# Performance work log

Hardware: AMD Instinct MI355X
Metric: run time of the kernel (lower is better)

## Reference

```python
import jax, jax.numpy as jnp
import numpy as np

NUM_ITEMS = 100000
OUT_DIM = 128
BATCH = 16384
HIST = 50
TOTAL = BATCH * HIST


def setup_inputs() -> dict:
    key = jax.random.key(0)
    k1, k2, k3, k4, k5, k6 = jax.random.split(key, 6)
    feature_ids = jax.random.randint(k1, (TOTAL,), 0, NUM_ITEMS + 1, dtype=jnp.int64 if jax.config.jax_enable_x64 else jnp.int32)
    # ratings in {0.5, 1.0, ..., 5.0} so that (r - 0.5) * 2 is an int index in [0, 10)
    ratings = jax.random.randint(k2, (TOTAL,), 0, 10).astype(jnp.float32) / 2.0 + 0.5
    segment_ids = jnp.repeat(jnp.arange(BATCH, dtype=jnp.int32), HIST)  # [TOTAL]
    item_ids = jax.random.randint(k3, (BATCH,), 0, NUM_ITEMS, dtype=jnp.int32)
    # kaiming_uniform_(a=sqrt(5)) on an [N, D] table -> U(-b, b) with b = sqrt(6 / ((1 + 5) * D)) = 1/sqrt(D)
    b = 1.0 / np.sqrt(OUT_DIM)
    user_W = jax.random.uniform(k4, (NUM_ITEMS + 1, OUT_DIM), jnp.float32, -b, b)
    rating_W = jax.random.uniform(k5, (10, OUT_DIM), jnp.float32, -b, b)
    item_W = jax.random.uniform(k6, (NUM_ITEMS, OUT_DIM), jnp.float32, -b, b)
    bias = jnp.zeros((OUT_DIM,), jnp.float32)
    return {"feature_ids": feature_ids, "ratings": ratings, "segment_ids": segment_ids,
            "item_ids": item_ids, "user_W": user_W, "rating_W": rating_W,
            "item_W": item_W, "bias": bias}


def reference(feature_ids, ratings, segment_ids, item_ids, user_W, rating_W, item_W, bias):
    batch = item_ids.shape[0]
    rating_idx = ((ratings - 0.5) * 2.0).astype(jnp.int32)          # [T], in [0, 10)
    rating_weights = rating_W[rating_idx]                            # [T, D] gather
    user_weights = user_W[feature_ids] * rating_weights              # [T, D] gather + multiply
    user_sum = jax.ops.segment_sum(user_weights, segment_ids, num_segments=batch)  # [B, D]
    return user_sum + item_W[item_ids] + bias                        # [B, D]
```

## Files before the change

### kernel.cpp

```cpp
#include <hip/hip_runtime.h>


#define BATCH     16384
#define HIST      50
#define DIM4      32
#define ROWS      8
#define BLOCK     256

__global__ __launch_bounds__(BLOCK) void features_linear_kernel(
    const int*    __restrict__ feature_ids,
    const float*  __restrict__ ratings,
    const int*    __restrict__ item_ids,
    const float4* __restrict__ user_W,
    const float4* __restrict__ rating_W,
    const float4* __restrict__ item_W,
    const float4* __restrict__ bias,
    float4*       __restrict__ out)
{
    __shared__ float4 sh_rW[10 * DIM4];
    __shared__ int    sh_fid[ROWS * HIST];
    __shared__ int    sh_ridx[ROWS * HIST];

    const int tid = threadIdx.x;

    for (int i = tid; i < 10 * DIM4; i += BLOCK) sh_rW[i] = rating_W[i];

    const int base = blockIdx.x * (ROWS * HIST);
    for (int i = tid; i < ROWS * HIST; i += BLOCK) {
        sh_fid[i] = feature_ids[base + i];
        float r = ratings[base + i];
        sh_ridx[i] = (int)(r * 2.0f) - 1;
    }
    __syncthreads();

    const int row = tid >> 5;
    const int d4  = tid & 31;
    const int b   = blockIdx.x * ROWS + row;

    float4 acc; acc.x = 0.f; acc.y = 0.f; acc.z = 0.f; acc.w = 0.f;
    const int off = row * HIST;

    for (int h = 0; h < HIST; ++h) {
        const int fid  = sh_fid[off + h];
        const int ridx = sh_ridx[off + h];
        const float4 u  = user_W[fid * DIM4 + d4];
        const float4 rw = sh_rW[ridx * DIM4 + d4];
        acc.x += u.x * rw.x;
        acc.y += u.y * rw.y;
        acc.z += u.z * rw.z;
        acc.w += u.w * rw.w;
    }

    const int iid = item_ids[b];
    const float4 iw = item_W[iid * DIM4 + d4];
    const float4 bs = bias[d4];

    float4 o;
    o.x = acc.x + iw.x + bs.x;
    o.y = acc.y + iw.y + bs.y;
    o.z = acc.z + iw.z + bs.z;
    o.w = acc.w + iw.w + bs.w;
    out[b * DIM4 + d4] = o;
}

extern "C" void kernel_launch(void* const* d_in, const int* in_sizes, int n_in,
                              void* d_out, int out_size, void* d_ws, size_t ws_size,
                              hipStream_t stream) {
    const int*    feature_ids = (const int*)   d_in[0];
    const float*  ratings     = (const float*) d_in[1];
    const int*    item_ids    = (const int*)   d_in[3];
    const float4* user_W      = (const float4*)d_in[4];
    const float4* rating_W    = (const float4*)d_in[5];
    const float4* item_W      = (const float4*)d_in[6];
    const float4* bias        = (const float4*)d_in[7];
    float4*       out         = (float4*)      d_out;

    dim3 grid(BATCH / ROWS);
    dim3 block(BLOCK);
    features_linear_kernel<<<grid, block, 0, stream>>>(
        feature_ids, ratings, item_ids, user_W, rating_W, item_W, bias, out);
}
```

Baseline: 173.0 us.

## Drop shared-memory staging and read ids and rating weights directly from global

Removes the LDS staging of rating_W, feature ids and rating indices along with the block barrier. Each half-wave now loads its ids and ratings straight from global memory inside the loop, which is unrolled by five, and gathers rating_W rows through the cache. Blocks shrink to 128 threads covering 4 rows, giving more, smaller blocks. The aim is to cut the prologue and sync cost and expose more memory-level parallelism, at the cost of redundant broadcast loads of ids and rating rows per lane.

```diff
diff --git a/kernel.cpp b/kernel.cpp
--- a/kernel.cpp
+++ b/kernel.cpp
@@ -1,11 +1,11 @@
 #include <hip/hip_runtime.h>
 
 
-#define BATCH     16384
-#define HIST      50
-#define DIM4      32
-#define ROWS      8
-#define BLOCK     256
+#define BATCH   16384
+#define HIST    50
+#define DIM4    32
+#define BLOCK   128
+#define ROWS_PER_BLOCK 4
 
 __global__ __launch_bounds__(BLOCK) void features_linear_kernel(
     const int*    __restrict__ feature_ids,
@@ -17,43 +17,35 @@
     const float4* __restrict__ bias,
     float4*       __restrict__ out)
 {
-    __shared__ float4 sh_rW[10 * DIM4];
-    __shared__ int    sh_fid[ROWS * HIST];
-    __shared__ int    sh_ridx[ROWS * HIST];
+    const int tid  = threadIdx.x;
+    const int wave = tid >> 6;
+    const int lane = tid & 63;
+    const int half = lane >> 5;
+    const int d4   = lane & 31;
 
-    const int tid = threadIdx.x;
+    const int b   = blockIdx.x * ROWS_PER_BLOCK + wave * 2 + half;
+    const int off = b * HIST;
 
-    for (int i = tid; i < 10 * DIM4; i += BLOCK) sh_rW[i] = rating_W[i];
-
-    const int base = blockIdx.x * (ROWS * HIST);
-    for (int i = tid; i < ROWS * HIST; i += BLOCK) {
-        sh_fid[i] = feature_ids[base + i];
-        float r = ratings[base + i];
-        sh_ridx[i] = (int)(r * 2.0f) - 1;
-    }
-    __syncthreads();
-
-    const int row = tid >> 5;
-    const int d4  = tid & 31;
-    const int b   = blockIdx.x * ROWS + row;
+    const int    iid = item_ids[b];
+    const float4 iw  = item_W[iid * DIM4 + d4];
+    const float4 bs  = bias[d4];
 
     float4 acc; acc.x = 0.f; acc.y = 0.f; acc.z = 0.f; acc.w = 0.f;
-    const int off = row * HIST;
 
+#pragma unroll 5
     for (int h = 0; h < HIST; ++h) {
-        const int fid  = sh_fid[off + h];
-        const int ridx = sh_ridx[off + h];
+        const int   fid  = feature_ids[off + h];
+        const float r    = ratings[off + h];
+        const int   ridx = (int)(r * 2.0f) - 1;
+
         const float4 u  = user_W[fid * DIM4 + d4];
-        const float4 rw = sh_rW[ridx * DIM4 + d4];
+        const float4 rw = rating_W[ridx * DIM4 + d4];
+
         acc.x += u.x * rw.x;
         acc.y += u.y * rw.y;
         acc.z += u.z * rw.z;
         acc.w += u.w * rw.w;
     }
-
-    const int iid = item_ids[b];
-    const float4 iw = item_W[iid * DIM4 + d4];
-    const float4 bs = bias[d4];
 
     float4 o;
     o.x = acc.x + iw.x + bs.x;
@@ -75,7 +67,7 @@
     const float4* bias        = (const float4*)d_in[7];
     float4*       out         = (float4*)      d_out;
 
-    dim3 grid(BATCH / ROWS);
+    dim3 grid(BATCH / ROWS_PER_BLOCK);
     dim3 block(BLOCK);
     features_linear_kernel<<<grid, block, 0, stream>>>(
         feature_ids, ratings, item_ids, user_W, rating_W, item_W, bias, out);
```

Measured after the change: 176.4 us. About the same (+2.0%).
